# Performance work log

Measured on AMD Instinct MI355X. Metric: run time of the kernel, lower is better.

The kernel has to match this reference:

```python
import jax, jax.numpy as jnp
import numpy as np
from jax import lax

SIGMA_D = 120.0
SIGMA_R = 1.2
WINDOW = 3
PAD = WINDOW // 2


def _sobel_kernels():
    smooth = jnp.array([1.0, 2.0, 1.0], dtype=jnp.float32) / 4.0
    deriv = jnp.array([1.0, 0.0, -1.0], dtype=jnp.float32)
    Kh = jnp.einsum('i,j,k->ijk', deriv, smooth, smooth)
    Kw = jnp.einsum('i,j,k->ijk', smooth, deriv, smooth)
    Kd = jnp.einsum('i,j,k->ijk', smooth, smooth, deriv)
    # (O=3, I=1, 3, 3, 3)
    return jnp.stack([Kh, Kw, Kd], axis=0)[:, None]


def _spatial_weights():
    r = np.arange(-PAD, PAD + 1)
    offs = np.stack(np.meshgrid(r, r, r, indexing='ij'), axis=-1).reshape(-1, 3).astype(np.float32)
    dist_sq = (offs ** 2).sum(axis=1)
    return jnp.asarray(np.exp(-dist_sq / (2.0 * SIGMA_D ** 2)))


def setup_inputs() -> dict:
    key = jax.random.key(0)
    volume = jax.random.normal(key, (1, 1, 96, 96, 96), dtype=jnp.float32)
    return {"volume": volume}


def reference(volume):
    B, C, D, H, W = volume.shape
    kernels = _sobel_kernels()
    # Sobel gradient, SAME (zero) padding like F.conv3d(padding=1): (B,3,D,H,W)
    grad = lax.conv_general_dilated(
        volume, kernels, window_strides=(1, 1, 1), padding=[(1, 1)] * 3,
        dimension_numbers=('NCDHW', 'OIDHW', 'NCDHW'))

    pad_cfg = ((0, 0), (0, 0), (PAD, PAD), (PAD, PAD), (PAD, PAD))
    vol_pad = jnp.pad(volume, pad_cfg, mode='edge')
    grad_pad = jnp.pad(grad, pad_cfg, mode='edge')

    offsets = [(dh, dw, dd) for dh in range(WINDOW) for dw in range(WINDOW) for dd in range(WINDOW)]
    # (B, K, D, H, W)
    neighbor_vals = jnp.stack(
        [vol_pad[:, 0, dh:dh + D, dw:dw + H, dd:dd + W] for (dh, dw, dd) in offsets], axis=1)
    # (B, K, 3, D, H, W)
    neighbor_grads = jnp.stack(
        [grad_pad[:, :, dh:dh + D, dw:dw + H, dd:dd + W] for (dh, dw, dd) in offsets], axis=1)

    # ||grad_p - grad_q||^2 over the 3 gradient channels; gaussian on the norm
    # equals exp(-||.||^2 / (2 sigma_r^2)) directly (sqrt then square cancels).
    grad_diff_sq = ((grad[:, None] - neighbor_grads) ** 2).sum(axis=2)  # (B,K,D,H,W)
    range_weights = jnp.exp(-grad_diff_sq / (2.0 * SIGMA_R ** 2))

    sw = _spatial_weights().reshape(1, -1, 1, 1, 1)
    weights = sw * range_weights
    numerator = (weights * neighbor_vals).sum(axis=1, keepdims=True)
    denominator = jnp.clip(weights.sum(axis=1, keepdims=True), 1e-8, None)
    return numerator / denominator
```

## Files before the change

kernel.cpp:

```cpp
#include <hip/hip_runtime.h>


#define NV 96
#define NV2 (NV * NV)

#define TX 32
#define TY 4
#define TZ 4
#define VX (TX + 4)
#define VY (TY + 4)
#define VZ (TZ + 4)
#define GX (TX + 2)
#define GY (TY + 2)
#define GZ (TZ + 2)

__global__ __launch_bounds__(256) void fused_bilateral_kernel(
    const float* __restrict__ vol, float* __restrict__ out) {
    __shared__ float sv[VZ][VY][VX];
    __shared__ float4 sq[GZ][GY][GX];

    const int X0 = blockIdx.x * TX;
    const int Y0 = blockIdx.y * TY;
    const int Z0 = blockIdx.z * TZ;
    const int t = threadIdx.x;

    for (int li = t; li < VX * VY * VZ; li += 256) {
        int lx = li % VX;
        int lyz = li / VX;
        int ly = lyz % VY;
        int lz = lyz / VY;
        int gx = X0 - 2 + lx;
        int gy = Y0 - 2 + ly;
        int gz = Z0 - 2 + lz;
        float v = 0.0f;
        if (gx >= 0 && gx < NV && gy >= 0 && gy < NV && gz >= 0 && gz < NV)
            v = vol[gz * NV2 + gy * NV + gx];
        sv[lz][ly][lx] = v;
    }
    __syncthreads();

    for (int li = t; li < GX * GY * GZ; li += 256) {
        int lx = li % GX;
        int lyz = li / GX;
        int ly = lyz % GY;
        int lz = lyz / GY;
        float gh = 0.0f, gw = 0.0f, gd = 0.0f;
#pragma unroll
        for (int a = 0; a < 3; ++a) {
            const float sma = (a == 1) ? 0.5f : 0.25f;
            const float dva = (a == 0) ? 1.0f : ((a == 2) ? -1.0f : 0.0f);
#pragma unroll
            for (int b = 0; b < 3; ++b) {
                const float smb = (b == 1) ? 0.5f : 0.25f;
                const float dvb = (b == 0) ? 1.0f : ((b == 2) ? -1.0f : 0.0f);
                float v0 = sv[lz + a][ly + b][lx + 0];
                float v1 = sv[lz + a][ly + b][lx + 1];
                float v2 = sv[lz + a][ly + b][lx + 2];
                float xs = 0.25f * v0 + 0.5f * v1 + 0.25f * v2;
                float xd = v0 - v2;
                gh += dva * smb * xs;
                gw += sma * dvb * xs;
                gd += sma * smb * xd;
            }
        }
        float cv = sv[lz + 1][ly + 1][lx + 1];
        sq[lz][ly][lx] = make_float4(gh, gw, gd, cv);
    }
    __syncthreads();

    const int tx = t & 31;
    const int ty = (t >> 5) & 3;
    const int tzh = t >> 7;

    const float inv2sd = 1.0f / (2.0f * 120.0f * 120.0f);
    const float inv2sr = 1.0f / (2.0f * 1.2f * 1.2f);

    const int ox = X0 + tx;
    const int oy = Y0 + ty;
    const int oz0 = Z0 + tzh;
    const int oz1 = oz0 + 2;

    const float4 c0 = sq[tzh + 1][ty + 1][tx + 1];
    const float4 c1 = sq[tzh + 3][ty + 1][tx + 1];

    int nx[3], ny[3], nz[5];
#pragma unroll
    for (int d = 0; d < 3; ++d) {
        nx[d] = min(max(ox + d - 1, 0), NV - 1) - (X0 - 1);
        ny[d] = min(max(oy + d - 1, 0), NV - 1) - (Y0 - 1);
    }
#pragma unroll
    for (int p = 0; p < 5; ++p)
        nz[p] = min(max(oz0 + p - 1, 0), NV - 1) - (Z0 - 1);

    float num0 = 0.0f, den0 = 0.0f, num1 = 0.0f, den1 = 0.0f;

#pragma unroll
    for (int p = 0; p < 5; ++p) {
#pragma unroll
        for (int iy = 0; iy < 3; ++iy) {
#pragma unroll
            for (int ix = 0; ix < 3; ++ix) {
                float4 q = sq[nz[p]][ny[iy]][nx[ix]];
                if (p <= 2) {
                    const float sdc =
                        (float)((p - 1) * (p - 1) + (iy - 1) * (iy - 1) +
                                (ix - 1) * (ix - 1)) * inv2sd;
                    float a = c0.x - q.x, b = c0.y - q.y, e = c0.z - q.z;
                    float g = a * a + b * b + e * e;
                    float w = __expf(-(sdc + g * inv2sr));
                    num0 += w * q.w;
                    den0 += w;
                }
                if (p >= 2) {
                    const float sdc =
                        (float)((p - 3) * (p - 3) + (iy - 1) * (iy - 1) +
                                (ix - 1) * (ix - 1)) * inv2sd;
                    float a = c1.x - q.x, b = c1.y - q.y, e = c1.z - q.z;
                    float g = a * a + b * b + e * e;
                    float w = __expf(-(sdc + g * inv2sr));
                    num1 += w * q.w;
                    den1 += w;
                }
            }
        }
    }

    out[oz0 * NV2 + oy * NV + ox] = num0 / fmaxf(den0, 1e-8f);
    out[oz1 * NV2 + oy * NV + ox] = num1 / fmaxf(den1, 1e-8f);
}

extern "C" void kernel_launch(void* const* d_in, const int* in_sizes, int n_in,
                              void* d_out, int out_size, void* d_ws, size_t ws_size,
                              hipStream_t stream) {
    const float* vol = (const float*)d_in[0];
    float* out = (float*)d_out;

    dim3 grid(NV / TX, NV / TY, NV / TZ);
    fused_bilateral_kernel<<<grid, dim3(256), 0, stream>>>(vol, out);
}
```

Baseline: 73.83 us.

## Enlarge tile, alias smem via union, compute gradient pairs, 4 z-outputs per thread

The tile grows to 32x8x4. The volume tile and the gradient tile now share one shared-memory union, with the gradient results held in registers across an extra barrier before they are written back. Each thread computes Sobel gradients for two adjacent x voxels so overlapping loads are reused. In the filter stage each thread handles a full z-column of 4 outputs, so each neighbor read from shared memory serves up to 3 outputs. This cuts shared-memory traffic and halo overhead per output, at the cost of higher register pressure, an added barrier, and a launch-bounds occupancy hint.

```diff
diff --git a/kernel.cpp b/kernel.cpp
--- a/kernel.cpp
+++ b/kernel.cpp
@@ -5,7 +5,7 @@
 #define NV2 (NV * NV)
 
 #define TX 32
-#define TY 4
+#define TY 8
 #define TZ 4
 #define VX (TX + 4)
 #define VY (TY + 4)
@@ -13,18 +13,22 @@
 #define GX (TX + 2)
 #define GY (TY + 2)
 #define GZ (TZ + 2)
+#define NVOL (VX * VY * VZ)
+#define NPAIR (GZ * GY * (GX / 2))
 
-__global__ __launch_bounds__(256) void fused_bilateral_kernel(
+__global__ __launch_bounds__(256, 4) void fused_bilateral_kernel(
     const float* __restrict__ vol, float* __restrict__ out) {
-    __shared__ float sv[VZ][VY][VX];
-    __shared__ float4 sq[GZ][GY][GX];
+    __shared__ union {
+        float sv[VZ][VY][VX];
+        float4 sq[GZ][GY][GX];
+    } u;
 
     const int X0 = blockIdx.x * TX;
     const int Y0 = blockIdx.y * TY;
     const int Z0 = blockIdx.z * TZ;
     const int t = threadIdx.x;
 
-    for (int li = t; li < VX * VY * VZ; li += 256) {
+    for (int li = t; li < NVOL; li += 256) {
         int lx = li % VX;
         int lyz = li / VX;
         int ly = lyz % VY;
@@ -35,16 +39,22 @@
         float v = 0.0f;
         if (gx >= 0 && gx < NV && gy >= 0 && gy < NV && gz >= 0 && gz < NV)
             v = vol[gz * NV2 + gy * NV + gx];
-        sv[lz][ly][lx] = v;
+        u.sv[lz][ly][lx] = v;
     }
     __syncthreads();
 
-    for (int li = t; li < GX * GY * GZ; li += 256) {
-        int lx = li % GX;
-        int lyz = li / GX;
-        int ly = lyz % GY;
-        int lz = lyz / GY;
-        float gh = 0.0f, gw = 0.0f, gd = 0.0f;
+    float4 r0[4], r1[4];
+#pragma unroll
+    for (int k = 0; k < 4; ++k) {
+        int li = t + k * 256;
+        int lp = (li < NPAIR) ? li : 0;
+        int lxp = lp % 17;
+        int lyy = (lp / 17) % GY;
+        int lzz = lp / (17 * GY);
+        int lx = lxp * 2;
+        float gh0 = 0.f, gw0 = 0.f, gd0 = 0.f;
+        float gh1 = 0.f, gw1 = 0.f, gd1 = 0.f;
+        float cv0 = 0.f, cv1 = 0.f;
 #pragma unroll
         for (int a = 0; a < 3; ++a) {
             const float sma = (a == 1) ? 0.5f : 0.25f;
@@ -53,81 +63,97 @@
             for (int b = 0; b < 3; ++b) {
                 const float smb = (b == 1) ? 0.5f : 0.25f;
                 const float dvb = (b == 0) ? 1.0f : ((b == 2) ? -1.0f : 0.0f);
-                float v0 = sv[lz + a][ly + b][lx + 0];
-                float v1 = sv[lz + a][ly + b][lx + 1];
-                float v2 = sv[lz + a][ly + b][lx + 2];
-                float xs = 0.25f * v0 + 0.5f * v1 + 0.25f * v2;
-                float xd = v0 - v2;
-                gh += dva * smb * xs;
-                gw += sma * dvb * xs;
-                gd += sma * smb * xd;
+                float v0 = u.sv[lzz + a][lyy + b][lx + 0];
+                float v1 = u.sv[lzz + a][lyy + b][lx + 1];
+                float v2 = u.sv[lzz + a][lyy + b][lx + 2];
+                float v3 = u.sv[lzz + a][lyy + b][lx + 3];
+                float xs0 = 0.25f * v0 + 0.5f * v1 + 0.25f * v2;
+                float xd0 = v0 - v2;
+                float xs1 = 0.25f * v1 + 0.5f * v2 + 0.25f * v3;
+                float xd1 = v1 - v3;
+                gh0 += dva * smb * xs0;
+                gw0 += sma * dvb * xs0;
+                gd0 += sma * smb * xd0;
+                gh1 += dva * smb * xs1;
+                gw1 += sma * dvb * xs1;
+                gd1 += sma * smb * xd1;
+                if (a == 1 && b == 1) { cv0 = v1; cv1 = v2; }
             }
         }
-        float cv = sv[lz + 1][ly + 1][lx + 1];
-        sq[lz][ly][lx] = make_float4(gh, gw, gd, cv);
+        r0[k] = make_float4(gh0, gw0, gd0, cv0);
+        r1[k] = make_float4(gh1, gw1, gd1, cv1);
+    }
+    __syncthreads();
+
+#pragma unroll
+    for (int k = 0; k < 4; ++k) {
+        int li = t + k * 256;
+        if (li < NPAIR) {
+            int lxp = li % 17;
+            int lyy = (li / 17) % GY;
+            int lzz = li / (17 * GY);
+            u.sq[lzz][lyy][lxp * 2] = r0[k];
+            u.sq[lzz][lyy][lxp * 2 + 1] = r1[k];
+        }
     }
     __syncthreads();
 
     const int tx = t & 31;
-    const int ty = (t >> 5) & 3;
-    const int tzh = t >> 7;
-
-    const float inv2sd = 1.0f / (2.0f * 120.0f * 120.0f);
-    const float inv2sr = 1.0f / (2.0f * 1.2f * 1.2f);
-
+    const int ty = t >> 5;
     const int ox = X0 + tx;
     const int oy = Y0 + ty;
-    const int oz0 = Z0 + tzh;
-    const int oz1 = oz0 + 2;
 
-    const float4 c0 = sq[tzh + 1][ty + 1][tx + 1];
-    const float4 c1 = sq[tzh + 3][ty + 1][tx + 1];
+    const float inv2sr = 1.0f / (2.0f * 1.2f * 1.2f);
+    const float inv2sd = 1.0f / (2.0f * 120.0f * 120.0f);
 
-    int nx[3], ny[3], nz[5];
+    const float4 c0 = u.sq[1][ty + 1][tx + 1];
+    const float4 c1 = u.sq[2][ty + 1][tx + 1];
+    const float4 c2 = u.sq[3][ty + 1][tx + 1];
+    const float4 c3 = u.sq[4][ty + 1][tx + 1];
+
+    int nx[3], ny[3], nz[6];
 #pragma unroll
     for (int d = 0; d < 3; ++d) {
         nx[d] = min(max(ox + d - 1, 0), NV - 1) - (X0 - 1);
         ny[d] = min(max(oy + d - 1, 0), NV - 1) - (Y0 - 1);
     }
 #pragma unroll
-    for (int p = 0; p < 5; ++p)
-        nz[p] = min(max(oz0 + p - 1, 0), NV - 1) - (Z0 - 1);
+    for (int p = 0; p < 6; ++p)
+        nz[p] = min(max(Z0 + p - 1, 0), NV - 1) - (Z0 - 1);
 
-    float num0 = 0.0f, den0 = 0.0f, num1 = 0.0f, den1 = 0.0f;
+    float num[4] = {0.f, 0.f, 0.f, 0.f};
+    float den[4] = {0.f, 0.f, 0.f, 0.f};
 
 #pragma unroll
-    for (int p = 0; p < 5; ++p) {
+    for (int p = 0; p < 6; ++p) {
 #pragma unroll
         for (int iy = 0; iy < 3; ++iy) {
 #pragma unroll
             for (int ix = 0; ix < 3; ++ix) {
-                float4 q = sq[nz[p]][ny[iy]][nx[ix]];
-                if (p <= 2) {
-                    const float sdc =
-                        (float)((p - 1) * (p - 1) + (iy - 1) * (iy - 1) +
-                                (ix - 1) * (ix - 1)) * inv2sd;
-                    float a = c0.x - q.x, b = c0.y - q.y, e = c0.z - q.z;
-                    float g = a * a + b * b + e * e;
-                    float w = __expf(-(sdc + g * inv2sr));
-                    num0 += w * q.w;
-                    den0 += w;
-                }
-                if (p >= 2) {
-                    const float sdc =
-                        (float)((p - 3) * (p - 3) + (iy - 1) * (iy - 1) +
-                                (ix - 1) * (ix - 1)) * inv2sd;
-                    float a = c1.x - q.x, b = c1.y - q.y, e = c1.z - q.z;
-                    float g = a * a + b * b + e * e;
-                    float w = __expf(-(sdc + g * inv2sr));
-                    num1 += w * q.w;
-                    den1 += w;
+                float4 q = u.sq[nz[p]][ny[iy]][nx[ix]];
+#pragma unroll
+                for (int k = 0; k < 4; ++k) {
+                    const int dz = p - 1 - k;
+                    if (dz >= -1 && dz <= 1) {
+                        const float SD =
+                            -(float)(dz * dz + (iy - 1) * (iy - 1) +
+                                     (ix - 1) * (ix - 1)) * inv2sd;
+                        float4 c = (k == 0) ? c0 : (k == 1) ? c1
+                                 : (k == 2) ? c2 : c3;
+                        float a = c.x - q.x, b = c.y - q.y, e = c.z - q.z;
+                        float g = a * a + b * b + e * e;
+                        float w = __expf(SD - g * inv2sr);
+                        num[k] += w * q.w;
+                        den[k] += w;
+                    }
                 }
             }
         }
     }
 
-    out[oz0 * NV2 + oy * NV + ox] = num0 / fmaxf(den0, 1e-8f);
-    out[oz1 * NV2 + oy * NV + ox] = num1 / fmaxf(den1, 1e-8f);
+#pragma unroll
+    for (int k = 0; k < 4; ++k)
+        out[(Z0 + k) * NV2 + oy * NV + ox] = num[k] / fmaxf(den[k], 1e-8f);
 }
 
 extern "C" void kernel_launch(void* const* d_in, const int* in_sizes, int n_in,
```

Measured after the change: 131.3 us. 77.8% more time.

## Compute Sobel gradients with a separable z-marching register pipeline

Applied to the files above, without the earlier changes.

Replaces the per-voxel 27-tap gradient loop with a column-per-thread sweep along z. Each thread computes separable xy partial sums per plane and keeps a three-plane rolling window in registers. This cuts shared-memory reads and redundant arithmetic in the gradient stage. Only 204 of 256 threads now work in this phase, and each runs a serial loop over 8 planes, so the stage loses parallelism and gains latency.

```diff
diff --git a/kernel.cpp b/kernel.cpp
--- a/kernel.cpp
+++ b/kernel.cpp
@@ -13,6 +13,7 @@
 #define GX (TX + 2)
 #define GY (TY + 2)
 #define GZ (TZ + 2)
+#define NVOL (VX * VY * VZ)
 
 __global__ __launch_bounds__(256) void fused_bilateral_kernel(
     const float* __restrict__ vol, float* __restrict__ out) {
@@ -24,7 +25,7 @@
     const int Z0 = blockIdx.z * TZ;
     const int t = threadIdx.x;
 
-    for (int li = t; li < VX * VY * VZ; li += 256) {
+    for (int li = t; li < NVOL; li += 256) {
         int lx = li % VX;
         int lyz = li / VX;
         int ly = lyz % VY;
@@ -39,32 +40,44 @@
     }
     __syncthreads();
 
-    for (int li = t; li < GX * GY * GZ; li += 256) {
-        int lx = li % GX;
-        int lyz = li / GX;
-        int ly = lyz % GY;
-        int lz = lyz / GY;
-        float gh = 0.0f, gw = 0.0f, gd = 0.0f;
+    if (t < GX * GY) {
+        const int gx_ = t % GX;
+        const int gy_ = t / GX;
+        float s0 = 0.f, s1 = 0.f, s2 = 0.f;
+        float w0 = 0.f, w1 = 0.f, w2 = 0.f;
+        float u0 = 0.f, u1 = 0.f, u2 = 0.f;
+        float v11p = 0.f;
 #pragma unroll
-        for (int a = 0; a < 3; ++a) {
-            const float sma = (a == 1) ? 0.5f : 0.25f;
-            const float dva = (a == 0) ? 1.0f : ((a == 2) ? -1.0f : 0.0f);
-#pragma unroll
-            for (int b = 0; b < 3; ++b) {
-                const float smb = (b == 1) ? 0.5f : 0.25f;
-                const float dvb = (b == 0) ? 1.0f : ((b == 2) ? -1.0f : 0.0f);
-                float v0 = sv[lz + a][ly + b][lx + 0];
-                float v1 = sv[lz + a][ly + b][lx + 1];
-                float v2 = sv[lz + a][ly + b][lx + 2];
-                float xs = 0.25f * v0 + 0.5f * v1 + 0.25f * v2;
-                float xd = v0 - v2;
-                gh += dva * smb * xs;
-                gw += sma * dvb * xs;
-                gd += sma * smb * xd;
+        for (int p = 0; p < VZ; ++p) {
+            float a00 = sv[p][gy_ + 0][gx_ + 0];
+            float a01 = sv[p][gy_ + 0][gx_ + 1];
+            float a02 = sv[p][gy_ + 0][gx_ + 2];
+            float a10 = sv[p][gy_ + 1][gx_ + 0];
+            float a11 = sv[p][gy_ + 1][gx_ + 1];
+            float a12 = sv[p][gy_ + 1][gx_ + 2];
+            float a20 = sv[p][gy_ + 2][gx_ + 0];
+            float a21 = sv[p][gy_ + 2][gx_ + 1];
+            float a22 = sv[p][gy_ + 2][gx_ + 2];
+            float r0 = 0.25f * a00 + 0.5f * a01 + 0.25f * a02;
+            float r1 = 0.25f * a10 + 0.5f * a11 + 0.25f * a12;
+            float r2 = 0.25f * a20 + 0.5f * a21 + 0.25f * a22;
+            float sxy = 0.25f * r0 + 0.5f * r1 + 0.25f * r2;
+            float dyx = r0 - r2;
+            float dx0 = a00 - a02;
+            float dx1 = a10 - a12;
+            float dx2 = a20 - a22;
+            float dxs = 0.25f * dx0 + 0.5f * dx1 + 0.25f * dx2;
+            s0 = s1; s1 = s2; s2 = sxy;
+            w0 = w1; w1 = w2; w2 = dyx;
+            u0 = u1; u1 = u2; u2 = dxs;
+            if (p >= 2) {
+                float gh = s0 - s2;
+                float gw = 0.25f * w0 + 0.5f * w1 + 0.25f * w2;
+                float gd = 0.25f * u0 + 0.5f * u1 + 0.25f * u2;
+                sq[p - 2][gy_][gx_] = make_float4(gh, gw, gd, v11p);
             }
+            v11p = a11;
         }
-        float cv = sv[lz + 1][ly + 1][lx + 1];
-        sq[lz][ly][lx] = make_float4(gh, gw, gd, cv);
     }
     __syncthreads();
 
```

Result: faster. 71.20 us (-3.6%).

## Split fused bilateral into separate Sobel-pack and bilateral kernels via workspace

Applied to the files above, without the earlier changes.

Replaces the single shared-memory-tiled fused kernel with two global-memory kernels. The first computes the Sobel gradient plus the center value into a float4 workspace, and the second gathers 27 float4 neighbors from global memory (relying on the cache) and uses exp2 with log2e folded into the constants. This removes the halo recomputation and the shared-memory barriers, but adds a 14 MB workspace round trip, a second launch, and uncoalesced float4 gathers.

```diff
diff --git a/kernel.cpp b/kernel.cpp
--- a/kernel.cpp
+++ b/kernel.cpp
@@ -3,131 +3,93 @@
 
 #define NV 96
 #define NV2 (NV * NV)
+#define NV3 (NV * NV * NV)
 
-#define TX 32
-#define TY 4
-#define TZ 4
-#define VX (TX + 4)
-#define VY (TY + 4)
-#define VZ (TZ + 4)
-#define GX (TX + 2)
-#define GY (TY + 2)
-#define GZ (TZ + 2)
+#define LOG2E 1.44269504088896340736f
 
-__global__ __launch_bounds__(256) void fused_bilateral_kernel(
-    const float* __restrict__ vol, float* __restrict__ out) {
-    __shared__ float sv[VZ][VY][VX];
-    __shared__ float4 sq[GZ][GY][GX];
+__global__ __launch_bounds__(256) void sobel_pack_kernel(
+    const float* __restrict__ vol, float4* __restrict__ gv) {
+    int idx = blockIdx.x * blockDim.x + threadIdx.x;
+    if (idx >= NV3) return;
+    int x = idx % NV;
+    int y = (idx / NV) % NV;
+    int z = idx / NV2;
 
-    const int X0 = blockIdx.x * TX;
-    const int Y0 = blockIdx.y * TY;
-    const int Z0 = blockIdx.z * TZ;
-    const int t = threadIdx.x;
+    float sz = 0.f, s1 = 0.f, s2 = 0.f;
+    (void)sz; (void)s1; (void)s2;
 
-    for (int li = t; li < VX * VY * VZ; li += 256) {
-        int lx = li % VX;
-        int lyz = li / VX;
-        int ly = lyz % VY;
-        int lz = lyz / VY;
-        int gx = X0 - 2 + lx;
-        int gy = Y0 - 2 + ly;
-        int gz = Z0 - 2 + lz;
-        float v = 0.0f;
-        if (gx >= 0 && gx < NV && gy >= 0 && gy < NV && gz >= 0 && gz < NV)
-            v = vol[gz * NV2 + gy * NV + gx];
-        sv[lz][ly][lx] = v;
+    float acc_ss = 0.f;
+    (void)acc_ss;
+
+    float gh = 0.f, gw = 0.f, gd = 0.f;
+#pragma unroll
+    for (int a = 0; a < 3; ++a) {
+        int zz = z + a - 1;
+        bool zok = (zz >= 0) && (zz < NV);
+        const float sma = (a == 1) ? 0.5f : 0.25f;
+        const float dva = (a == 0) ? 1.0f : ((a == 2) ? -1.0f : 0.0f);
+#pragma unroll
+        for (int b = 0; b < 3; ++b) {
+            int yy = y + b - 1;
+            bool rok = zok && (yy >= 0) && (yy < NV);
+            const float smb = (b == 1) ? 0.5f : 0.25f;
+            const float dvb = (b == 0) ? 1.0f : ((b == 2) ? -1.0f : 0.0f);
+            int rowbase = zz * NV2 + yy * NV + x;
+            float v0 = (rok && x >= 1) ? vol[rowbase - 1] : 0.f;
+            float v1 = rok ? vol[rowbase] : 0.f;
+            float v2 = (rok && x < NV - 1) ? vol[rowbase + 1] : 0.f;
+            float xs = 0.25f * v0 + 0.5f * v1 + 0.25f * v2;
+            float xd = v0 - v2;
+            gh += dva * smb * xs;
+            gw += sma * dvb * xs;
+            gd += sma * smb * xd;
+        }
     }
-    __syncthreads();
+    gv[idx] = make_float4(gh, gw, gd, vol[idx]);
+}
 
-    for (int li = t; li < GX * GY * GZ; li += 256) {
-        int lx = li % GX;
-        int lyz = li / GX;
-        int ly = lyz % GY;
-        int lz = lyz / GY;
-        float gh = 0.0f, gw = 0.0f, gd = 0.0f;
-#pragma unroll
-        for (int a = 0; a < 3; ++a) {
-            const float sma = (a == 1) ? 0.5f : 0.25f;
-            const float dva = (a == 0) ? 1.0f : ((a == 2) ? -1.0f : 0.0f);
-#pragma unroll
-            for (int b = 0; b < 3; ++b) {
-                const float smb = (b == 1) ? 0.5f : 0.25f;
-                const float dvb = (b == 0) ? 1.0f : ((b == 2) ? -1.0f : 0.0f);
-                float v0 = sv[lz + a][ly + b][lx + 0];
-                float v1 = sv[lz + a][ly + b][lx + 1];
-                float v2 = sv[lz + a][ly + b][lx + 2];
-                float xs = 0.25f * v0 + 0.5f * v1 + 0.25f * v2;
-                float xd = v0 - v2;
-                gh += dva * smb * xs;
-                gw += sma * dvb * xs;
-                gd += sma * smb * xd;
-            }
-        }
-        float cv = sv[lz + 1][ly + 1][lx + 1];
-        sq[lz][ly][lx] = make_float4(gh, gw, gd, cv);
-    }
-    __syncthreads();
+__global__ __launch_bounds__(256) void bilateral_kernel(
+    const float4* __restrict__ gv, float* __restrict__ out) {
+    int idx = blockIdx.x * blockDim.x + threadIdx.x;
+    if (idx >= NV3) return;
+    int x = idx % NV;
+    int y = (idx / NV) % NV;
+    int z = idx / NV2;
 
-    const int tx = t & 31;
-    const int ty = (t >> 5) & 3;
-    const int tzh = t >> 7;
+    const float RC = LOG2E / (2.0f * 1.2f * 1.2f);
 
-    const float inv2sd = 1.0f / (2.0f * 120.0f * 120.0f);
-    const float inv2sr = 1.0f / (2.0f * 1.2f * 1.2f);
+    float4 c = gv[idx];
 
-    const int ox = X0 + tx;
-    const int oy = Y0 + ty;
-    const int oz0 = Z0 + tzh;
-    const int oz1 = oz0 + 2;
-
-    const float4 c0 = sq[tzh + 1][ty + 1][tx + 1];
-    const float4 c1 = sq[tzh + 3][ty + 1][tx + 1];
-
-    int nx[3], ny[3], nz[5];
+    int nx[3], ny[3], nz[3];
 #pragma unroll
     for (int d = 0; d < 3; ++d) {
-        nx[d] = min(max(ox + d - 1, 0), NV - 1) - (X0 - 1);
-        ny[d] = min(max(oy + d - 1, 0), NV - 1) - (Y0 - 1);
+        nx[d] = min(max(x + d - 1, 0), NV - 1);
+        ny[d] = min(max(y + d - 1, 0), NV - 1);
+        nz[d] = min(max(z + d - 1, 0), NV - 1);
     }
+
+    float num = 0.f, den = 0.f;
 #pragma unroll
-    for (int p = 0; p < 5; ++p)
-        nz[p] = min(max(oz0 + p - 1, 0), NV - 1) - (Z0 - 1);
-
-    float num0 = 0.0f, den0 = 0.0f, num1 = 0.0f, den1 = 0.0f;
-
+    for (int a = 0; a < 3; ++a) {
 #pragma unroll
-    for (int p = 0; p < 5; ++p) {
+        for (int b = 0; b < 3; ++b) {
+            int rowbase = nz[a] * NV2 + ny[b] * NV;
 #pragma unroll
-        for (int iy = 0; iy < 3; ++iy) {
-#pragma unroll
-            for (int ix = 0; ix < 3; ++ix) {
-                float4 q = sq[nz[p]][ny[iy]][nx[ix]];
-                if (p <= 2) {
-                    const float sdc =
-                        (float)((p - 1) * (p - 1) + (iy - 1) * (iy - 1) +
-                                (ix - 1) * (ix - 1)) * inv2sd;
-                    float a = c0.x - q.x, b = c0.y - q.y, e = c0.z - q.z;
-                    float g = a * a + b * b + e * e;
-                    float w = __expf(-(sdc + g * inv2sr));
-                    num0 += w * q.w;
-                    den0 += w;
-                }
-                if (p >= 2) {
-                    const float sdc =
-                        (float)((p - 3) * (p - 3) + (iy - 1) * (iy - 1) +
-                                (ix - 1) * (ix - 1)) * inv2sd;
-                    float a = c1.x - q.x, b = c1.y - q.y, e = c1.z - q.z;
-                    float g = a * a + b * b + e * e;
-                    float w = __expf(-(sdc + g * inv2sr));
-                    num1 += w * q.w;
-                    den1 += w;
-                }
+            for (int d = 0; d < 3; ++d) {
+                const float SDC =
+                    -(float)((a - 1) * (a - 1) + (b - 1) * (b - 1) +
+                             (d - 1) * (d - 1)) *
+                    (LOG2E / (2.0f * 120.0f * 120.0f));
+                float4 q = gv[rowbase + nx[d]];
+                float dx_ = c.x - q.x, dy_ = c.y - q.y, dz_ = c.z - q.z;
+                float g = dx_ * dx_ + dy_ * dy_ + dz_ * dz_;
+                float w = __builtin_amdgcn_exp2f(fmaf(-g, RC, SDC));
+                num += w * q.w;
+                den += w;
             }
         }
     }
-
-    out[oz0 * NV2 + oy * NV + ox] = num0 / fmaxf(den0, 1e-8f);
-    out[oz1 * NV2 + oy * NV + ox] = num1 / fmaxf(den1, 1e-8f);
+    out[idx] = num / fmaxf(den, 1e-8f);
 }
 
 extern "C" void kernel_launch(void* const* d_in, const int* in_sizes, int n_in,
@@ -135,7 +97,11 @@
                               hipStream_t stream) {
     const float* vol = (const float*)d_in[0];
     float* out = (float*)d_out;
+    float4* gv = (float4*)d_ws;
 
-    dim3 grid(NV / TX, NV / TY, NV / TZ);
-    fused_bilateral_kernel<<<grid, dim3(256), 0, stream>>>(vol, out);
+    const int threads = 256;
+    const int blocks = (NV3 + threads - 1) / threads;
+
+    sobel_pack_kernel<<<blocks, threads, 0, stream>>>(vol, gv);
+    bilateral_kernel<<<blocks, threads, 0, stream>>>(gv, out);
 }
```

Measured after the change: 80.82 us. 1.09x slower.
